# Kernel optimization log

Measured on AMD Instinct MI355X. Metric: run time of the kernel, lower is better.

Reference implementation:

```python
import jax, jax.numpy as jnp
import numpy as np

N, E, B = 8000, 128000, 16
DIN, D, H, C, L = 16, 256, 8, 32, 6
MC, NT = 200, 8
NEG_SLOPE = 0.2


def layernorm(x, s, b):
    mu = jnp.mean(x, axis=-1, keepdims=True)
    var = jnp.mean(jnp.square(x - mu), axis=-1, keepdims=True)
    return (x - mu) * jax.lax.rsqrt(var + 1e-5) * s + b


def setup_inputs() -> dict:
    key = jax.random.key(0)
    ks = iter(jax.random.split(key, 64))
    rn = lambda shape, s=0.05: jax.random.normal(next(ks), shape, jnp.float32) * s
    inp = {}
    inp['x'] = jax.random.normal(next(ks), (N, DIN), jnp.float32)
    inp['edge_index'] = jax.random.randint(next(ks), (2, E), 0, N)
    inp['batch'] = jnp.sort(jax.random.randint(next(ks), (N,), 0, B))
    # node encoder: Linear(DIN,D) + LayerNorm
    inp['enc_W'] = rn((DIN, D)); inp['enc_b'] = jnp.zeros((D,), jnp.float32)
    inp['enc_ls'] = jnp.ones((D,), jnp.float32); inp['enc_lb'] = jnp.zeros((D,), jnp.float32)
    # GATv2 layers (stacked): lin_l, lin_r, att, output bias, post LayerNorm
    inp['Wl'] = rn((L, D, D)); inp['bl'] = jnp.zeros((L, D), jnp.float32)
    inp['Wr'] = rn((L, D, D)); inp['br'] = jnp.zeros((L, D), jnp.float32)
    inp['att'] = rn((L, H, C))
    inp['gb'] = jnp.zeros((L, D), jnp.float32)
    inp['gls'] = jnp.ones((L, D), jnp.float32); inp['glb'] = jnp.zeros((L, D), jnp.float32)
    # color head MLP: D -> D -> D//2 -> MC
    inp['cW1'] = rn((D, D)); inp['cb1'] = jnp.zeros((D,), jnp.float32)
    inp['cW2'] = rn((D, D // 2)); inp['cb2'] = jnp.zeros((D // 2,), jnp.float32)
    inp['cW3'] = rn((D // 2, MC)); inp['cb3'] = jnp.zeros((MC,), jnp.float32)
    # chromatic head: 2D -> D -> D//2 -> MC
    inp['chW1'] = rn((2 * D, D)); inp['chb1'] = jnp.zeros((D,), jnp.float32)
    inp['chW2'] = rn((D, D // 2)); inp['chb2'] = jnp.zeros((D // 2,), jnp.float32)
    inp['chW3'] = rn((D // 2, MC)); inp['chb3'] = jnp.zeros((MC,), jnp.float32)
    # type head: 2D -> 128 -> NT
    inp['tW1'] = rn((2 * D, 128)); inp['tb1'] = jnp.zeros((128,), jnp.float32)
    inp['tW2'] = rn((128, NT)); inp['tb2'] = jnp.zeros((NT,), jnp.float32)
    # difficulty head: 2D -> 64 -> 1, sigmoid * 100
    inp['dW1'] = rn((2 * D, 64)); inp['db1'] = jnp.zeros((64,), jnp.float32)
    inp['dW2'] = rn((64, 1)); inp['db2'] = jnp.zeros((1,), jnp.float32)
    return inp


def reference(x, edge_index, batch, enc_W, enc_b, enc_ls, enc_lb,
              Wl, bl, Wr, br, att, gb, gls, glb,
              cW1, cb1, cW2, cb2, cW3, cb3,
              chW1, chb1, chW2, chb2, chW3, chb3,
              tW1, tb1, tW2, tb2, dW1, db1, dW2, db2):
    n = x.shape[0]
    # node encoder (dropout = identity at inference)
    h = jax.nn.relu(layernorm(x @ enc_W + enc_b, enc_ls, enc_lb))
    # add self loops once (same for every layer)
    sl = jnp.arange(n)
    src = jnp.concatenate([edge_index[0], sl])  # message source j
    dst = jnp.concatenate([edge_index[1], sl])  # message target i
    for i in range(L):
        xl = (h @ Wl[i] + bl[i]).reshape(n, H, C)  # source transform
        xr = (h @ Wr[i] + br[i]).reshape(n, H, C)  # target transform
        # GATv2 attention: a^T LeakyReLU(xl_j + xr_i)
        e = jax.nn.leaky_relu(xl[src] + xr[dst], NEG_SLOPE)  # [E+N, H, C]
        logits = jnp.einsum('ehc,hc->eh', e, att[i])          # [E+N, H]
        # segment softmax over destination node (self-loops guarantee denom > 0)
        m = jax.ops.segment_max(logits, dst, num_segments=n)
        m = jnp.where(jnp.isfinite(m), m, 0.0)
        p = jnp.exp(logits - m[dst])
        denom = jax.ops.segment_sum(p, dst, num_segments=n)
        alpha = p / denom[dst]
        out = jax.ops.segment_sum(xl[src] * alpha[:, :, None], dst, num_segments=n)
        out = out.reshape(n, D) + gb[i]
        h_new = jax.nn.elu(layernorm(out, gls[i], glb[i]))
        h = h + h_new if i > 0 else h_new
    # per-node color logits
    z = jax.nn.relu(h @ cW1 + cb1)
    z = jax.nn.relu(z @ cW2 + cb2)
    node_colors = z @ cW3 + cb3
    # global mean/max pooling per graph
    cnt = jax.ops.segment_sum(jnp.ones((n,), h.dtype), batch, num_segments=B)
    mean_p = jax.ops.segment_sum(h, batch, num_segments=B) / jnp.maximum(cnt, 1.0)[:, None]
    max_p = jax.ops.segment_max(h, batch, num_segments=B)
    max_p = jnp.where(jnp.isfinite(max_p), max_p, 0.0)
    g = jnp.concatenate([mean_p, max_p], axis=1)  # [B, 2D]
    zc = jax.nn.relu(g @ chW1 + chb1)
    zc = jax.nn.relu(zc @ chW2 + chb2)
    chromatic_num = zc @ chW3 + chb3
    zt = jax.nn.relu(g @ tW1 + tb1)
    graph_type = zt @ tW2 + tb2
    zd = jax.nn.relu(g @ dW1 + db1)
    difficulty = jax.nn.sigmoid(zd @ dW2 + db2) * 100.0
    return (node_colors, chromatic_num, graph_type, difficulty)
```

## Files before the change

kernel.cpp:

```cpp
#include <hip/hip_runtime.h>
#include <hip/hip_bf16.h>

constexpr int DIN = 16;
constexpr int D   = 256;
constexpr int NH  = 8;
constexpr int NC  = 32;
constexpr int MC  = 200;
constexpr int NT  = 8;
constexpr int BG  = 16;
constexpr int NL  = 6;
constexpr int PS  = 16;
constexpr float NEG = 0.2f;

typedef __attribute__((ext_vector_type(8))) short bfrag;
typedef __attribute__((ext_vector_type(4))) float f32x4;

__device__ inline unsigned short f2bf(float f) {
    unsigned int u = __float_as_uint(f);
    u += 0x7FFFu + ((u >> 16) & 1u);
    return (unsigned short)(u >> 16);
}
__device__ inline float bf2f(unsigned short u) {
    return __uint_as_float((unsigned int)u << 16);
}

__device__ inline float dot_ilp(const float* g, const float* __restrict__ W, int K, int ldw, int t) {
    float a0 = 0.f, a1 = 0.f, a2 = 0.f, a3 = 0.f;
    for (int k = 0; k < K; k += 4) {
        a0 = fmaf(g[k + 0], W[(k + 0) * ldw + t], a0);
        a1 = fmaf(g[k + 1], W[(k + 1) * ldw + t], a1);
        a2 = fmaf(g[k + 2], W[(k + 2) * ldw + t], a2);
        a3 = fmaf(g[k + 3], W[(k + 3) * ldw + t], a3);
    }
    return (a0 + a1) + (a2 + a3);
}


__device__ inline void enc_node(const float* x, const float* W, const float* b, const float* ls,
                                const float* lb, float* h, int n, int lane) {
    int c4 = lane * 4;
    float xs[DIN];
#pragma unroll
    for (int k = 0; k < DIN; k += 4) {
        float4 xv = *(const float4*)&x[n * DIN + k];
        xs[k] = xv.x; xs[k + 1] = xv.y; xs[k + 2] = xv.z; xs[k + 3] = xv.w;
    }
    float4 a = *(const float4*)&b[c4];
#pragma unroll
    for (int k = 0; k < DIN; k++) {
        float4 wv = *(const float4*)&W[k * D + c4];
        a.x = fmaf(xs[k], wv.x, a.x);
        a.y = fmaf(xs[k], wv.y, a.y);
        a.z = fmaf(xs[k], wv.z, a.z);
        a.w = fmaf(xs[k], wv.w, a.w);
    }
    float s = a.x + a.y + a.z + a.w;
#pragma unroll
    for (int msk = 1; msk <= 32; msk <<= 1) s += __shfl_xor(s, msk);
    float mu = s * (1.f / D);
    float4 dv = make_float4(a.x - mu, a.y - mu, a.z - mu, a.w - mu);
    float v2 = dv.x * dv.x + dv.y * dv.y + dv.z * dv.z + dv.w * dv.w;
#pragma unroll
    for (int msk = 1; msk <= 32; msk <<= 1) v2 += __shfl_xor(v2, msk);
    float rstd = rsqrtf(v2 * (1.f / D) + 1e-5f);
    float4 lsv = *(const float4*)&ls[c4];
    float4 lbv = *(const float4*)&lb[c4];
    float4 y = make_float4(fmaxf(dv.x * rstd * lsv.x + lbv.x, 0.f),
                           fmaxf(dv.y * rstd * lsv.y + lbv.y, 0.f),
                           fmaxf(dv.z * rstd * lsv.z + lbv.z, 0.f),
                           fmaxf(dv.w * rstd * lsv.w + lbv.w, 0.f));
    *(float4*)&h[(size_t)n * D + c4] = y;
}

__device__ inline float4 attn_compute(const unsigned short* xl, const unsigned short* xr,
                                      const int* row_ptr, const int* col, const float* att,
                                      const float* gb, const float* gls, const float* glb,
                                      const float* h, int layer, int n, int lane) {
    int c4 = lane * 4;
    ushort4 xr4 = *(const ushort4*)&xr[(size_t)n * D + c4];
    float4 xrv = make_float4(bf2f(xr4.x), bf2f(xr4.y), bf2f(xr4.z), bf2f(xr4.w));
    float4 av  = *(const float4*)&att[c4];
    int beg = row_ptr[n], end = row_ptr[n + 1];
    int deg = end - beg;
    int myc = col[beg + min(lane, deg - 1)];
    float l = 0.f;
    float4 acc = make_float4(0.f, 0.f, 0.f, 0.f);
    auto loadx = [&](int i) -> ushort4 {
        if (i < deg) {
            int s = (i < 64) ? __shfl(myc, i) : col[beg + i];
            return *(const ushort4*)&xl[(size_t)s * D + c4];
        }
        return make_ushort4(0, 0, 0, 0);
    };
    auto step = [&](ushort4 x4) {
        float4 xlv = make_float4(bf2f(x4.x), bf2f(x4.y), bf2f(x4.z), bf2f(x4.w));
        float sx = xlv.x + xrv.x; sx = sx > 0.f ? sx : NEG * sx;
        float sy = xlv.y + xrv.y; sy = sy > 0.f ? sy : NEG * sy;
        float sz = xlv.z + xrv.z; sz = sz > 0.f ? sz : NEG * sz;
        float sw = xlv.w + xrv.w; sw = sw > 0.f ? sw : NEG * sw;
        float z = av.x * sx + av.y * sy + av.z * sz + av.w * sw;
        z += __shfl_xor(z, 1); z += __shfl_xor(z, 2); z += __shfl_xor(z, 4);
        float p = __expf(z);
        l += p;
        acc.x = fmaf(p, xlv.x, acc.x);
        acc.y = fmaf(p, xlv.y, acc.y);
        acc.z = fmaf(p, xlv.z, acc.z);
        acc.w = fmaf(p, xlv.w, acc.w);
    };
    ushort4 b0 = loadx(0), b1 = loadx(1), b2 = loadx(2), b3 = loadx(3);
    int e = 0;
    for (; e + 4 <= deg; e += 4) {
        ushort4 n0 = loadx(e + 4), n1 = loadx(e + 5), n2 = loadx(e + 6), n3 = loadx(e + 7);
        step(b0); step(b1); step(b2); step(b3);
        b0 = n0; b1 = n1; b2 = n2; b3 = n3;
    }
    if (e + 0 < deg) step(b0);
    if (e + 1 < deg) step(b1);
    if (e + 2 < deg) step(b2);
    float4 gbv = *(const float4*)&gb[c4];
    float rl = 1.f / l;
    float4 o = make_float4(acc.x * rl + gbv.x, acc.y * rl + gbv.y,
                           acc.z * rl + gbv.z, acc.w * rl + gbv.w);
    float s = o.x + o.y + o.z + o.w;
#pragma unroll
    for (int msk = 1; msk <= 32; msk <<= 1) s += __shfl_xor(s, msk);
    float mu = s * (1.f / D);
    float4 dv = make_float4(o.x - mu, o.y - mu, o.z - mu, o.w - mu);
    float v2 = dv.x * dv.x + dv.y * dv.y + dv.z * dv.z + dv.w * dv.w;
#pragma unroll
    for (int msk = 1; msk <= 32; msk <<= 1) v2 += __shfl_xor(v2, msk);
    float rstd = rsqrtf(v2 * (1.f / D) + 1e-5f);
    float4 glsv = *(const float4*)&gls[c4];
    float4 glbv = *(const float4*)&glb[c4];
    float y0 = dv.x * rstd * glsv.x + glbv.x;
    float y1 = dv.y * rstd * glsv.y + glbv.y;
    float y2 = dv.z * rstd * glsv.z + glbv.z;
    float y3 = dv.w * rstd * glsv.w + glbv.w;
    y0 = y0 > 0.f ? y0 : expm1f(y0);
    y1 = y1 > 0.f ? y1 : expm1f(y1);
    y2 = y2 > 0.f ? y2 : expm1f(y2);
    y3 = y3 > 0.f ? y3 : expm1f(y3);
    float4 prev = make_float4(0.f, 0.f, 0.f, 0.f);
    if (layer > 0) prev = *(const float4*)&h[(size_t)n * D + c4];
    return make_float4(prev.x + y0, prev.y + y1, prev.z + y2, prev.w + y3);
}

__device__ inline void gemm_one_ct(const unsigned short (*As)[264],
                                   const unsigned short* WpL, const unsigned short* WpR,
                                   const float* bl, const float* br,
                                   unsigned short* xl, unsigned short* xr,
                                   int N, int nb, int ctg, int lane) {
    int m = lane & 15, q = lane >> 4;
    float bLv = bl[ctg * 16 + m];
    float bRv = br[ctg * 16 + m];
    f32x4 accL = (f32x4){bLv, bLv, bLv, bLv};
    f32x4 accR = (f32x4){bRv, bRv, bRv, bRv};
#pragma unroll
    for (int ks = 0; ks < 8; ks++) {
        bfrag af = *(const bfrag*)&As[m][ks * 32 + q * 8];
        size_t off = (((size_t)ctg * 8 + ks) * 64 + lane) * 8;
        bfrag bL = *(const bfrag*)&WpL[off];
        bfrag bR = *(const bfrag*)&WpR[off];
        accL = __builtin_amdgcn_mfma_f32_16x16x32_bf16(af, bL, accL, 0, 0, 0);
        accR = __builtin_amdgcn_mfma_f32_16x16x32_bf16(af, bR, accR, 0, 0, 0);
    }
    int colg = ctg * 16 + m;
#pragma unroll
    for (int reg = 0; reg < 4; reg++) {
        int row = nb + q * 4 + reg;
        if (row < N) {
            xl[(size_t)row * D + colg] = f2bf(accL[reg]);
            xr[(size_t)row * D + colg] = f2bf(accR[reg]);
        }
    }
}

__device__ inline void gemm_core(const unsigned short (*As)[264],
                                 const unsigned short* WpL, const unsigned short* WpR,
                                 const float* bl, const float* br,
                                 unsigned short* xl, unsigned short* xr, int N, int nb, int T) {
    int lane = T & 63, w = T >> 6;
#pragma unroll
    for (int ct = 0; ct < 4; ct++)
        gemm_one_ct(As, WpL, WpR, bl, br, xl, xr, N, nb, w * 4 + ct, lane);
}

__device__ inline void repack_attn_one(const float* Wl, const float* Wr, unsigned short* Wp, int tid) {
    int lane = tid & 63;
    int r1 = tid >> 6;
    int ks = r1 & 7;
    int r2 = r1 >> 3;
    int ct = r2 & 15;
    int mi = r2 >> 4;
    int layer = mi >> 1, mat = mi & 1;
    const float* W = (mat == 0 ? Wl : Wr) + (size_t)layer * D * D;
    int n = ct * 16 + (lane & 15);
    int kb = ks * 32 + (lane >> 4) * 8;
    size_t base = (((size_t)(mi * 16 + ct) * 8 + ks) * 64 + lane) * 8;
#pragma unroll
    for (int j = 0; j < 8; j++) Wp[base + j] = f2bf(W[(size_t)(kb + j) * D + n]);
}

__device__ inline void repack_gen_one(const float* W, unsigned short* Wp, int K, int NCOL, int nks, int tid) {
    int lane = tid & 63;
    int r = tid >> 6;
    int ks = r % nks;
    int ct = r / nks;
    int n = ct * 16 + (lane & 15);
    int kb = ks * 32 + (lane >> 4) * 8;
    size_t base = (((size_t)ct * nks + ks) * 64 + lane) * 8;
#pragma unroll
    for (int j = 0; j < 8; j++) {
        int k = kb + j;
        Wp[base + j] = (n < NCOL && k < K) ? f2bf(W[(size_t)k * NCOL + n]) : (unsigned short)0;
    }
}


__global__ __launch_bounds__(256) void init_enc_k(const float* __restrict__ x, const float* __restrict__ W,
                                                  const float* __restrict__ b, const float* __restrict__ ls,
                                                  const float* __restrict__ lb, float* __restrict__ h,
                                                  int* __restrict__ deg, int N) {
    int gid = blockIdx.x * 256 + threadIdx.x;
    if (gid < N) deg[gid] = 1;
    int lane = threadIdx.x & 63;
    int n = blockIdx.x * 4 + (threadIdx.x >> 6);
    if (n < N) enc_node(x, W, b, ls, lb, h, n, lane);
}

__global__ __launch_bounds__(256) void count_repack_k(const int* __restrict__ dst, int* __restrict__ deg, int E,
                                                      const float* __restrict__ Wl, const float* __restrict__ Wr,
                                                      unsigned short* __restrict__ Wp,
                                                      const float* __restrict__ cW1, unsigned short* __restrict__ cW1p,
                                                      const float* __restrict__ cW2, unsigned short* __restrict__ cW2p,
                                                      const float* __restrict__ cW3, unsigned short* __restrict__ cW3p) {
    int gid = blockIdx.x * 256 + threadIdx.x;
    if (gid < E) atomicAdd(&deg[dst[gid]], 1);
    if (gid < NL * 2 * 16 * 8 * 64) repack_attn_one(Wl, Wr, Wp, gid);
    if (gid < 16 * 8 * 64) repack_gen_one(cW1, cW1p, D, D, 8, gid);
    if (gid < 8 * 8 * 64)  repack_gen_one(cW2, cW2p, D, 128, 8, gid);
    if (gid < 13 * 4 * 64) repack_gen_one(cW3, cW3p, 128, MC, 4, gid);
}

__global__ __launch_bounds__(1024) void scan_k(const int* __restrict__ deg, int* __restrict__ row_ptr,
                                               int* __restrict__ fill, int N) {
    __shared__ int sd[1024];
    int t = threadIdx.x;
    int chunk = (N + 1023) >> 10;
    int lo = t * chunk, hi = min(lo + chunk, N);
    int s = 0;
    for (int i = lo; i < hi; i++) s += deg[i];
    sd[t] = s;
    __syncthreads();
    for (int off = 1; off < 1024; off <<= 1) {
        int v = (t >= off) ? sd[t - off] : 0;
        __syncthreads();
        sd[t] += v;
        __syncthreads();
    }
    int run = (t > 0) ? sd[t - 1] : 0;
    for (int i = lo; i < hi; i++) {
        row_ptr[i] = run; fill[i] = run;
        run += deg[i];
    }
    if (t == 1023) row_ptr[N] = sd[1023];
}

__global__ __launch_bounds__(256) void scatter_gemm0_k(const int* __restrict__ src, const int* __restrict__ dst,
                                                       int* __restrict__ fill, int* __restrict__ col, int E, int N,
                                                       const float* __restrict__ h,
                                                       const unsigned short* __restrict__ WpL,
                                                       const unsigned short* __restrict__ WpR,
                                                       const float* __restrict__ bl, const float* __restrict__ br,
                                                       unsigned short* __restrict__ xl, unsigned short* __restrict__ xr) {
    __shared__ unsigned short As[16][264];
    int T = threadIdx.x;
    int tt = blockIdx.x;
    int ntiles = (N + 15) >> 4;
    if (tt < ntiles) {
        int nb = tt * 16;
#pragma unroll
        for (int r = 0; r < 16; r++) {
            int row = nb + r;
            float v = (row < N) ? h[(size_t)row * D + T] : 0.f;
            As[r][T] = f2bf(v);
        }
        __syncthreads();
        gemm_core(As, WpL, WpR, bl, br, xl, xr, N, nb, T);
    }
    for (int e = blockIdx.x * 256 + T; e < E + N; e += gridDim.x * 256) {
        if (e < E) {
            int p = atomicAdd(&fill[dst[e]], 1);
            col[p] = src[e];
        } else {
            int n = e - E;
            int p = atomicAdd(&fill[n], 1);
            col[p] = n;
        }
    }
}

__global__ __launch_bounds__(256, 8) void attn_k(const unsigned short* __restrict__ xl_in,
                                                 const unsigned short* __restrict__ xr_in,
                                                 const int* __restrict__ row_ptr, const int* __restrict__ col,
                                                 const float* __restrict__ att, const float* __restrict__ gb,
                                                 const float* __restrict__ gls, const float* __restrict__ glb,
                                                 float* __restrict__ h, int layer, int N) {
    int T = threadIdx.x;
    int lane = T & 63, wv = T >> 6;
    int n = blockIdx.x * 4 + wv;
    if (n >= N) return;
    float4 res = attn_compute(xl_in, xr_in, row_ptr, col, att, gb, gls, glb, h, layer, n, lane);
    *(float4*)&h[(size_t)n * D + lane * 4] = res;
}

__global__ __launch_bounds__(256, 4) void gemm_lr_k(const float* __restrict__ h,
                                                    const unsigned short* __restrict__ WpL,
                                                    const unsigned short* __restrict__ WpR,
                                                    const float* __restrict__ bl, const float* __restrict__ br,
                                                    unsigned short* __restrict__ xl, unsigned short* __restrict__ xr,
                                                    int N) {
    __shared__ unsigned short As[16][264];
    int T = threadIdx.x;
    int nb = blockIdx.x * 16;
#pragma unroll
    for (int r = 0; r < 16; r++) {
        int row = nb + r;
        float v = (row < N) ? h[(size_t)row * D + T] : 0.f;
        As[r][T] = f2bf(v);
    }
    __syncthreads();
    gemm_core(As, WpL, WpR, bl, br, xl, xr, N, nb, T);
}

__global__ __launch_bounds__(1024) void colorhead_k(const float* __restrict__ h, int N,
                                                    const unsigned short* __restrict__ W1p, const float* __restrict__ b1,
                                                    const unsigned short* __restrict__ W2p, const float* __restrict__ b2,
                                                    const unsigned short* __restrict__ W3p, const float* __restrict__ b3,
                                                    float* __restrict__ out) {
    __shared__ unsigned short As[16][264];
    __shared__ unsigned short Zs[16][264];
    int T = threadIdx.x;
    int lane = T & 63, wv = T >> 6;
    int nb = blockIdx.x * 16;
    int c4 = lane * 4;
    int n = nb + wv;
    if (n < N) {
        float4 v = *(const float4*)&h[(size_t)n * D + c4];
        As[wv][c4 + 0] = f2bf(v.x);
        As[wv][c4 + 1] = f2bf(v.y);
        As[wv][c4 + 2] = f2bf(v.z);
        As[wv][c4 + 3] = f2bf(v.w);
    } else {
        As[wv][c4 + 0] = 0; As[wv][c4 + 1] = 0; As[wv][c4 + 2] = 0; As[wv][c4 + 3] = 0;
    }
    __syncthreads();
    int m = lane & 15, q = lane >> 4;
    {
        float bv = b1[wv * 16 + m];
        f32x4 acc = (f32x4){bv, bv, bv, bv};
#pragma unroll
        for (int ks = 0; ks < 8; ks++) {
            bfrag af = *(const bfrag*)&As[m][ks * 32 + q * 8];
            bfrag bf = *(const bfrag*)&W1p[(((size_t)wv * 8 + ks) * 64 + lane) * 8];
            acc = __builtin_amdgcn_mfma_f32_16x16x32_bf16(af, bf, acc, 0, 0, 0);
        }
        int colg = wv * 16 + m;
#pragma unroll
        for (int reg = 0; reg < 4; reg++)
            Zs[q * 4 + reg][colg] = f2bf(fmaxf(acc[reg], 0.f));
    }
    __syncthreads();
    if (wv < 8) {
        float bv = b2[wv * 16 + m];
        f32x4 acc = (f32x4){bv, bv, bv, bv};
#pragma unroll
        for (int ks = 0; ks < 8; ks++) {
            bfrag af = *(const bfrag*)&Zs[m][ks * 32 + q * 8];
            bfrag bf = *(const bfrag*)&W2p[(((size_t)wv * 8 + ks) * 64 + lane) * 8];
            acc = __builtin_amdgcn_mfma_f32_16x16x32_bf16(af, bf, acc, 0, 0, 0);
        }
        int colg = wv * 16 + m;
#pragma unroll
        for (int reg = 0; reg < 4; reg++)
            As[q * 4 + reg][colg] = f2bf(fmaxf(acc[reg], 0.f));
    }
    __syncthreads();
    if (wv < 13) {
        int colg = wv * 16 + m;
        float bv = (colg < MC) ? b3[colg] : 0.f;
        f32x4 acc = (f32x4){bv, bv, bv, bv};
#pragma unroll
        for (int ks = 0; ks < 4; ks++) {
            bfrag af = *(const bfrag*)&As[m][ks * 32 + q * 8];
            bfrag bf = *(const bfrag*)&W3p[(((size_t)wv * 4 + ks) * 64 + lane) * 8];
            acc = __builtin_amdgcn_mfma_f32_16x16x32_bf16(af, bf, acc, 0, 0, 0);
        }
#pragma unroll
        for (int reg = 0; reg < 4; reg++) {
            int row = nb + q * 4 + reg;
            if (row < N && colg < MC) out[(size_t)row * MC + colg] = acc[reg];
        }
    }
}

__global__ __launch_bounds__(256) void pool_k(const float* __restrict__ h, const int* __restrict__ batch,
                                              float* __restrict__ psum, float* __restrict__ pmax,
                                              int* __restrict__ cnt, int N) {
    int b = blockIdx.x;
    int sl = blockIdx.y;
    int c = threadIdx.x;
    int lo = 0, hi = N;
    while (lo < hi) { int mid = (lo + hi) >> 1; if (batch[mid] < b) lo = mid + 1; else hi = mid; }
    int s0 = lo;
    lo = 0; hi = N;
    while (lo < hi) { int mid = (lo + hi) >> 1; if (batch[mid] < b + 1) lo = mid + 1; else hi = mid; }
    int s1 = lo;
    int len = s1 - s0;
    int chunk = (len + PS - 1) / PS;
    int n0 = s0 + sl * chunk;
    int n1 = min(n0 + chunk, s1);
    float sum = 0.f, mx = -3.0e38f;
    for (int n = n0; n < n1; n++) {
        float v = h[(size_t)n * D + c];
        sum += v;
        mx = fmaxf(mx, v);
    }
    psum[(size_t)(b * PS + sl) * D + c] = sum;
    pmax[(size_t)(b * PS + sl) * D + c] = mx;
    if (c == 0 && sl == 0) cnt[b] = len;
}

__global__ __launch_bounds__(256) void heads_k(const float* __restrict__ psum, const float* __restrict__ pmax,
                                               const int* __restrict__ cnt,
                                               const float* __restrict__ chW1, const float* __restrict__ chb1,
                                               const float* __restrict__ chW2, const float* __restrict__ chb2,
                                               const float* __restrict__ chW3, const float* __restrict__ chb3,
                                               const float* __restrict__ tW1, const float* __restrict__ tb1,
                                               const float* __restrict__ tW2, const float* __restrict__ tb2,
                                               const float* __restrict__ dW1, const float* __restrict__ db1,
                                               const float* __restrict__ dW2, const float* __restrict__ db2,
                                               float* __restrict__ out_ch, float* __restrict__ out_t,
                                               float* __restrict__ out_d) {
    int b = blockIdx.x, sec = blockIdx.y, t = threadIdx.x;
    __shared__ float g[2 * D];
    __shared__ float z1[D];
    __shared__ float z2[128];
    float sum = 0.f, mx = -3.0e38f;
#pragma unroll
    for (int sl = 0; sl < PS; sl++) {
        sum += psum[(size_t)(b * PS + sl) * D + t];
        mx = fmaxf(mx, pmax[(size_t)(b * PS + sl) * D + t]);
    }
    int cn = cnt[b];
    float c = fmaxf((float)cn, 1.f);
    g[t] = sum / c;
    g[D + t] = (cn > 0) ? mx : 0.f;
    __syncthreads();
    if (sec == 0) {
        z1[t] = fmaxf(chb1[t] + dot_ilp(g, chW1, 2 * D, D, t), 0.f);
        __syncthreads();
        if (t < 128) z2[t] = fmaxf(chb2[t] + dot_ilp(z1, chW2, D, 128, t), 0.f);
        __syncthreads();
        if (t < MC) out_ch[b * MC + t] = chb3[t] + dot_ilp(z2, chW3, 128, MC, t);
    } else if (sec == 1) {
        if (t < 128) z1[t] = fmaxf(tb1[t] + dot_ilp(g, tW1, 2 * D, 128, t), 0.f);
        __syncthreads();
        if (t < NT) out_t[b * NT + t] = tb2[t] + dot_ilp(z1, tW2, 128, NT, t);
    } else {
        if (t < 64) z1[t] = fmaxf(db1[t] + dot_ilp(g, dW1, 2 * D, 64, t), 0.f);
        __syncthreads();
        if (t == 0) {
            float a = db2[0] + dot_ilp(z1, dW2, 64, 1, 0);
            out_d[b] = 100.f / (1.f + __expf(-a));
        }
    }
}

extern "C" void kernel_launch(void* const* d_in, const int* in_sizes, int n_in,
                              void* d_out, int out_size, void* d_ws, size_t ws_size,
                              hipStream_t stream) {
    const float* x     = (const float*)d_in[0];
    const int*   ei    = (const int*)d_in[1];
    const int*   batch = (const int*)d_in[2];
    const float* encW  = (const float*)d_in[3];
    const float* encb  = (const float*)d_in[4];
    const float* encls = (const float*)d_in[5];
    const float* enclb = (const float*)d_in[6];
    const float* Wl    = (const float*)d_in[7];
    const float* bl    = (const float*)d_in[8];
    const float* Wr    = (const float*)d_in[9];
    const float* br    = (const float*)d_in[10];
    const float* att   = (const float*)d_in[11];
    const float* gb    = (const float*)d_in[12];
    const float* gls   = (const float*)d_in[13];
    const float* glb   = (const float*)d_in[14];
    const float* cW1   = (const float*)d_in[15];
    const float* cb1   = (const float*)d_in[16];
    const float* cW2   = (const float*)d_in[17];
    const float* cb2   = (const float*)d_in[18];
    const float* cW3   = (const float*)d_in[19];
    const float* cb3   = (const float*)d_in[20];
    const float* chW1  = (const float*)d_in[21];
    const float* chb1  = (const float*)d_in[22];
    const float* chW2  = (const float*)d_in[23];
    const float* chb2  = (const float*)d_in[24];
    const float* chW3  = (const float*)d_in[25];
    const float* chb3  = (const float*)d_in[26];
    const float* tW1   = (const float*)d_in[27];
    const float* tb1   = (const float*)d_in[28];
    const float* tW2   = (const float*)d_in[29];
    const float* tb2   = (const float*)d_in[30];
    const float* dW1   = (const float*)d_in[31];
    const float* db1   = (const float*)d_in[32];
    const float* dW2   = (const float*)d_in[33];
    const float* db2   = (const float*)d_in[34];

    const int N = in_sizes[0] / DIN;
    const int E = in_sizes[1] / 2;
    const int* esrc = ei;
    const int* edst = ei + E;

    char* p = (char*)d_ws;
    auto carve = [&](size_t bytes) { char* r = p; p += (bytes + 255) & ~(size_t)255; return r; };
    int*            row_ptr = (int*)carve((size_t)(N + 1) * 4);
    int*            fill    = (int*)carve((size_t)N * 4);
    int*            deg     = (int*)carve((size_t)N * 4);
    int*            cnt     = (int*)carve((size_t)BG * 4);
    float*          psum    = (float*)carve((size_t)BG * PS * D * 4);
    float*          pmax    = (float*)carve((size_t)BG * PS * D * 4);
    int*            col     = (int*)carve((size_t)(E + N) * 4);
    unsigned short* Wp      = (unsigned short*)carve((size_t)NL * 2 * 65536 * 2);
    unsigned short* cW1p    = (unsigned short*)carve((size_t)16 * 8 * 64 * 8 * 2);
    unsigned short* cW2p    = (unsigned short*)carve((size_t)8 * 8 * 64 * 8 * 2);
    unsigned short* cW3p    = (unsigned short*)carve((size_t)13 * 4 * 64 * 8 * 2);
    float*          h       = (float*)carve((size_t)N * D * 4);
    unsigned short* xlA     = (unsigned short*)carve((size_t)N * D * 2);
    unsigned short* xrA     = (unsigned short*)carve((size_t)N * D * 2);
    unsigned short* xlB     = (unsigned short*)carve((size_t)N * D * 2);
    unsigned short* xrB     = (unsigned short*)carve((size_t)N * D * 2);
    (void)ws_size; (void)n_in; (void)out_size;

    const int ntiles16 = (N + 15) / 16;
    const int nblk4    = (N + 3) / 4;
    const int sblocks = max(ntiles16, (E + N + 255) / 256);

    init_enc_k<<<(N + 3) / 4, 256, 0, stream>>>(x, encW, encb, encls, enclb, h, deg, N);
    count_repack_k<<<512, 256, 0, stream>>>(edst, deg, E, Wl, Wr, Wp, cW1, cW1p, cW2, cW2p, cW3, cW3p);
    scan_k<<<1, 1024, 0, stream>>>(deg, row_ptr, fill, N);
    scatter_gemm0_k<<<sblocks, 256, 0, stream>>>(esrc, edst, fill, col, E, N, h,
                                                 Wp + 0, Wp + (size_t)65536,
                                                 bl + 0, br + 0, xlA, xrA);
    for (int l = 0; l < NL - 1; l++) {
        const unsigned short* xin_l = (l & 1) ? xlB : xlA;
        const unsigned short* xin_r = (l & 1) ? xrB : xrA;
        unsigned short* xout_l = (l & 1) ? xlA : xlB;
        unsigned short* xout_r = (l & 1) ? xrA : xrB;
        attn_k<<<nblk4, 256, 0, stream>>>(xin_l, xin_r, row_ptr, col, att + l * NH * NC,
                                          gb + l * D, gls + l * D, glb + l * D, h, l, N);
        gemm_lr_k<<<ntiles16, 256, 0, stream>>>(h,
                                                Wp + (size_t)((l + 1) * 2 + 0) * 65536,
                                                Wp + (size_t)((l + 1) * 2 + 1) * 65536,
                                                bl + (l + 1) * D, br + (l + 1) * D, xout_l, xout_r, N);
    }
    float* out = (float*)d_out;
    attn_k<<<nblk4, 256, 0, stream>>>(xlB, xrB, row_ptr, col, att + (NL - 1) * NH * NC,
                                      gb + (NL - 1) * D, gls + (NL - 1) * D, glb + (NL - 1) * D,
                                      h, NL - 1, N);
    colorhead_k<<<ntiles16, 1024, 0, stream>>>(h, N, cW1p, cb1, cW2p, cb2, cW3p, cb3, out);
    pool_k<<<dim3(BG, PS), 256, 0, stream>>>(h, batch, psum, pmax, cnt, N);
    heads_k<<<dim3(BG, 3), 256, 0, stream>>>(psum, pmax, cnt, chW1, chb1, chW2, chb2, chW3, chb3,
                                             tW1, tb1, tW2, tb2, dW1, db1, dW2, db2,
                                             out + (size_t)N * MC,
                                             out + (size_t)N * MC + BG * MC,
                                             out + (size_t)N * MC + BG * MC + BG * NT);
}
```

Before: 419.8 us.

## Fuse encoder and degree/repack kernels, deepen attention edge prefetch

Merges the node encoder kernel with the degree-count and weight-repack kernel, replacing the in-kernel degree init with a memset and adding the self-loop +1 inside the scan. The attention edge loop now keeps eight gathered rows in flight instead of four, with staggered reloads, and its occupancy hint drops from 8 to 6 blocks to make room for the extra registers. This aims to cut one launch and hide more gather latency, at the cost of register pressure and an added memset.

```diff
diff --git a/kernel.cpp b/kernel.cpp
--- a/kernel.cpp
+++ b/kernel.cpp
@@ -108,15 +108,25 @@
         acc.w = fmaf(p, xlv.w, acc.w);
     };
     ushort4 b0 = loadx(0), b1 = loadx(1), b2 = loadx(2), b3 = loadx(3);
+    ushort4 b4 = loadx(4), b5 = loadx(5), b6 = loadx(6), b7 = loadx(7);
     int e = 0;
-    for (; e + 4 <= deg; e += 4) {
-        ushort4 n0 = loadx(e + 4), n1 = loadx(e + 5), n2 = loadx(e + 6), n3 = loadx(e + 7);
-        step(b0); step(b1); step(b2); step(b3);
-        b0 = n0; b1 = n1; b2 = n2; b3 = n3;
+    for (; e + 8 <= deg; e += 8) {
+        step(b0); b0 = loadx(e + 8);
+        step(b1); b1 = loadx(e + 9);
+        step(b2); b2 = loadx(e + 10);
+        step(b3); b3 = loadx(e + 11);
+        step(b4); b4 = loadx(e + 12);
+        step(b5); b5 = loadx(e + 13);
+        step(b6); b6 = loadx(e + 14);
+        step(b7); b7 = loadx(e + 15);
     }
     if (e + 0 < deg) step(b0);
     if (e + 1 < deg) step(b1);
     if (e + 2 < deg) step(b2);
+    if (e + 3 < deg) step(b3);
+    if (e + 4 < deg) step(b4);
+    if (e + 5 < deg) step(b5);
+    if (e + 6 < deg) step(b6);
     float4 gbv = *(const float4*)&gb[c4];
     float rl = 1.f / l;
     float4 o = make_float4(acc.x * rl + gbv.x, acc.y * rl + gbv.y,
@@ -217,24 +227,19 @@
 }
 
 
-__global__ __launch_bounds__(256) void init_enc_k(const float* __restrict__ x, const float* __restrict__ W,
-                                                  const float* __restrict__ b, const float* __restrict__ ls,
-                                                  const float* __restrict__ lb, float* __restrict__ h,
-                                                  int* __restrict__ deg, int N) {
+__global__ __launch_bounds__(256) void fused_init_k(const float* __restrict__ x, const float* __restrict__ encW,
+                                                    const float* __restrict__ encb, const float* __restrict__ encls,
+                                                    const float* __restrict__ enclb, float* __restrict__ h, int N,
+                                                    const int* __restrict__ dst, int* __restrict__ deg, int E,
+                                                    const float* __restrict__ Wl, const float* __restrict__ Wr,
+                                                    unsigned short* __restrict__ Wp,
+                                                    const float* __restrict__ cW1, unsigned short* __restrict__ cW1p,
+                                                    const float* __restrict__ cW2, unsigned short* __restrict__ cW2p,
+                                                    const float* __restrict__ cW3, unsigned short* __restrict__ cW3p) {
     int gid = blockIdx.x * 256 + threadIdx.x;
-    if (gid < N) deg[gid] = 1;
     int lane = threadIdx.x & 63;
     int n = blockIdx.x * 4 + (threadIdx.x >> 6);
-    if (n < N) enc_node(x, W, b, ls, lb, h, n, lane);
-}
-
-__global__ __launch_bounds__(256) void count_repack_k(const int* __restrict__ dst, int* __restrict__ deg, int E,
-                                                      const float* __restrict__ Wl, const float* __restrict__ Wr,
-                                                      unsigned short* __restrict__ Wp,
-                                                      const float* __restrict__ cW1, unsigned short* __restrict__ cW1p,
-                                                      const float* __restrict__ cW2, unsigned short* __restrict__ cW2p,
-                                                      const float* __restrict__ cW3, unsigned short* __restrict__ cW3p) {
-    int gid = blockIdx.x * 256 + threadIdx.x;
+    if (n < N) enc_node(x, encW, encb, encls, enclb, h, n, lane);
     if (gid < E) atomicAdd(&deg[dst[gid]], 1);
     if (gid < NL * 2 * 16 * 8 * 64) repack_attn_one(Wl, Wr, Wp, gid);
     if (gid < 16 * 8 * 64) repack_gen_one(cW1, cW1p, D, D, 8, gid);
@@ -249,7 +254,7 @@
     int chunk = (N + 1023) >> 10;
     int lo = t * chunk, hi = min(lo + chunk, N);
     int s = 0;
-    for (int i = lo; i < hi; i++) s += deg[i];
+    for (int i = lo; i < hi; i++) s += deg[i] + 1;
     sd[t] = s;
     __syncthreads();
     for (int off = 1; off < 1024; off <<= 1) {
@@ -261,7 +266,7 @@
     int run = (t > 0) ? sd[t - 1] : 0;
     for (int i = lo; i < hi; i++) {
         row_ptr[i] = run; fill[i] = run;
-        run += deg[i];
+        run += deg[i] + 1;
     }
     if (t == 1023) row_ptr[N] = sd[1023];
 }
@@ -300,7 +305,7 @@
     }
 }
 
-__global__ __launch_bounds__(256, 8) void attn_k(const unsigned short* __restrict__ xl_in,
+__global__ __launch_bounds__(256, 6) void attn_k(const unsigned short* __restrict__ xl_in,
                                                  const unsigned short* __restrict__ xr_in,
                                                  const int* __restrict__ row_ptr, const int* __restrict__ col,
                                                  const float* __restrict__ att, const float* __restrict__ gb,
@@ -543,10 +548,13 @@
 
     const int ntiles16 = (N + 15) / 16;
     const int nblk4    = (N + 3) / 4;
-    const int sblocks = max(ntiles16, (E + N + 255) / 256);
-
-    init_enc_k<<<(N + 3) / 4, 256, 0, stream>>>(x, encW, encb, encls, enclb, h, deg, N);
-    count_repack_k<<<512, 256, 0, stream>>>(edst, deg, E, Wl, Wr, Wp, cW1, cW1p, cW2, cW2p, cW3, cW3p);
+    const int sblocks  = max(ntiles16, (E + N + 255) / 256);
+    const int fblocks  = max((N + 3) / 4, max((E + 255) / 256, 384));
+
+    hipMemsetAsync(deg, 0, (size_t)N * 4, stream);
+    fused_init_k<<<fblocks, 256, 0, stream>>>(x, encW, encb, encls, enclb, h, N,
+                                              edst, deg, E, Wl, Wr, Wp,
+                                              cW1, cW1p, cW2, cW2p, cW3, cW3p);
     scan_k<<<1, 1024, 0, stream>>>(deg, row_ptr, fill, N);
     scatter_gemm0_k<<<sblocks, 256, 0, stream>>>(esrc, edst, fill, col, E, N, h,
                                                  Wp + 0, Wp + (size_t)65536,
```

After: 501.2 us. +19.4%, slower.
